# Kernel tuning notes

Measured on AMD Instinct MI355X. Metric: run time of the kernel, lower is better.

The kernel has to match this reference:

```python
import jax, jax.numpy as jnp
import numpy as np

N_NODES = 50000
N_EDGES = 1600000
NUM_REL = 4
IN_F = 256
OUT_F = 128


def setup_inputs() -> dict:
    key = jax.random.key(0)
    k1, k2, k3 = jax.random.split(key, 3)
    X = jax.random.normal(k1, (N_NODES, IN_F), dtype=jnp.float32)
    # Glorot-ish scale for the per-relation GraphConv weights
    W = jax.random.normal(k2, (NUM_REL, IN_F, OUT_F), dtype=jnp.float32) * (1.0 / np.sqrt(IN_F))
    edge_index = jax.random.randint(k3, (NUM_REL, 2, N_EDGES), 0, N_NODES, dtype=jnp.int64 if jax.config.jax_enable_x64 else jnp.int32)
    return {"X": X, "W": W, "edge_index": edge_index}


def _graph_conv(X, Wr, src, dst, n_nodes):
    """DGL GraphConv, norm='both', bias=False, allow_zero_in_degree=True."""
    ones = jnp.ones(src.shape, dtype=X.dtype)
    out_deg = jax.ops.segment_sum(ones, src, num_segments=n_nodes)
    in_deg = jax.ops.segment_sum(ones, dst, num_segments=n_nodes)
    out_norm = jnp.clip(out_deg, 1.0, None) ** -0.5  # [N]
    in_norm = jnp.clip(in_deg, 1.0, None) ** -0.5    # [N]
    # in_feats > out_feats: apply weight first (same math, cheaper messages)
    h = (X * out_norm[:, None]) @ Wr                 # [N, out]
    agg = jax.ops.segment_sum(h[src], dst, num_segments=n_nodes)  # [N, out]
    return agg * in_norm[:, None]


def reference(X, W, edge_index):
    n_nodes = X.shape[0]
    num_rel = W.shape[0]
    Z = jnp.zeros((n_nodes, W.shape[2]), dtype=X.dtype)
    for r in range(num_rel):  # small fixed loop over relations
        Z = Z + _graph_conv(X, W[r], edge_index[r, 0], edge_index[r, 1], n_nodes)
    return Z
```

## Files before the change

### kernel.cpp

```cpp
#include <hip/hip_runtime.h>

#define IN_F 256
#define OUT_F 128
#define NUM_REL 4
#define BN 64
#define PBX 64
#define PT 512

typedef unsigned int u32;
typedef unsigned short u16;
typedef unsigned char u8;

typedef __attribute__((ext_vector_type(8))) short bf16x8;
typedef __attribute__((ext_vector_type(4))) float f32x4;

static __device__ __forceinline__ u16 f32_to_bf16(float f) {
    union { float f; u32 u; } c; c.f = f;
    u32 u = c.u;
    u32 r = (u + 0x7fffu + ((u >> 16) & 1u)) >> 16;
    return (u16)r;
}
static __device__ __forceinline__ float bf16lo(u32 v) {
    union { u32 u; float f; } c; c.u = v << 16; return c.f;
}
static __device__ __forceinline__ float bf16hi(u32 v) {
    union { u32 u; float f; } c; c.u = v & 0xffff0000u; return c.f;
}

__global__ __launch_bounds__(PT) void p1_hist(const int* __restrict__ EI, u32* __restrict__ ghd,
                                              u32* __restrict__ ghs, int E, int NB, int r0) {
    int rr = blockIdx.y, x = blockIdx.x;
    int r = r0 + rr;
    const int* src = EI + (size_t)(2 * r) * E;
    const int* dst = src + E;
    extern __shared__ u32 sh[];
    u32* hd = sh; u32* hs = sh + NB;
    for (int i = threadIdx.x; i < 2 * NB; i += PT) sh[i] = 0;
    __syncthreads();
    int CH = (E + PBX - 1) / PBX;
    int lo = x * CH, hi = min(E, lo + CH);
    for (int e = lo + threadIdx.x; e < hi; e += PT) {
        atomicAdd(&hd[dst[e] >> 6], 1u);
        atomicAdd(&hs[src[e] >> 6], 1u);
    }
    __syncthreads();
    for (int b = threadIdx.x; b < NB; b += PT) {
        ghd[(size_t)(rr * NB + b) * PBX + x] = hd[b];
        ghs[(size_t)(rr * NB + b) * PBX + x] = hs[b];
    }
}

__global__ __launch_bounds__(256) void p2a_scan(u32* __restrict__ ghd, u32* __restrict__ ghs,
                                                u32* __restrict__ bintot, int BINS) {
    int wid = blockIdx.x * 4 + (threadIdx.x >> 6);
    int lane = threadIdx.x & 63;
    if (wid >= 2 * BINS) return;
    u32* g = (wid < BINS) ? ghd : ghs;
    int bin = (wid < BINS) ? wid : wid - BINS;
    u32 c = g[(size_t)bin * PBX + lane];
    u32 xv = c;
    #pragma unroll
    for (int s = 1; s < 64; s <<= 1) {
        u32 y = __shfl_up(xv, s);
        if (lane >= s) xv += y;
    }
    g[(size_t)bin * PBX + lane] = xv - c;
    if (lane == 63) bintot[wid] = xv;
}

__global__ __launch_bounds__(1024) void p2b_scan(const u32* __restrict__ bintot,
                                                 u32* __restrict__ binbase_d,
                                                 u32* __restrict__ binbase_s, int BINS) {
    __shared__ u32 s[1024];
    __shared__ u32 carry;
    int t = threadIdx.x;
    for (int seg = 0; seg < 2; seg++) {
        const u32* in = bintot + (size_t)seg * BINS;
        u32* out = seg ? binbase_s : binbase_d;
        if (t == 0) carry = 0;
        __syncthreads();
        for (int base = 0; base < BINS; base += 1024) {
            int i = base + t;
            u32 v = (i < BINS) ? in[i] : 0;
            s[t] = v;
            __syncthreads();
            for (int off = 1; off < 1024; off <<= 1) {
                u32 x = (t >= off) ? s[t - off] : 0;
                __syncthreads();
                s[t] += x;
                __syncthreads();
            }
            u32 incl = s[t]; u32 c0 = carry;
            if (i < BINS) out[i] = c0 + incl - v;
            __syncthreads();
            if (t == 1023) carry = c0 + incl;
            __syncthreads();
        }
        if (t == 0) out[BINS] = carry;
        __syncthreads();
    }
}

__global__ __launch_bounds__(PT) void p3_scatter(const int* __restrict__ EI,
                                                 const u32* __restrict__ ghd, const u32* __restrict__ ghs,
                                                 const u32* __restrict__ binbase_d, const u32* __restrict__ binbase_s,
                                                 u32* __restrict__ part_dst, u8* __restrict__ part_src,
                                                 int E, int NB, int r0) {
    int rr = blockIdx.y, x = blockIdx.x;
    int r = r0 + rr;
    const int* src = EI + (size_t)(2 * r) * E;
    const int* dst = src + E;
    extern __shared__ u32 sh[];
    u32* base_d = sh; u32* cur_d = sh + NB; u32* base_s = sh + 2 * NB; u32* cur_s = sh + 3 * NB;
    for (int b = threadIdx.x; b < NB; b += PT) {
        int bin = rr * NB + b;
        base_d[b] = binbase_d[bin] + ghd[(size_t)bin * PBX + x];
        base_s[b] = binbase_s[bin] + ghs[(size_t)bin * PBX + x];
        cur_d[b] = 0; cur_s[b] = 0;
    }
    __syncthreads();
    int CH = (E + PBX - 1) / PBX;
    int lo = x * CH, hi = min(E, lo + CH);
    for (int e = lo + threadIdx.x; e < hi; e += PT) {
        int sv = src[e], dv = dst[e];
        int db = dv >> 6, sb = sv >> 6;
        u32 rk = atomicAdd(&cur_d[db], 1u);
        part_dst[base_d[db] + rk] = ((u32)sv << 6) | (u32)(dv & 63);
        u32 rk2 = atomicAdd(&cur_s[sb], 1u);
        part_src[base_s[sb] + rk2] = (u8)(sv & 63);
    }
}

__global__ __launch_bounds__(256) void srccount_kernel(const u8* __restrict__ part_src,
                                                       const u32* __restrict__ binbase_s,
                                                       float* __restrict__ out_norm, int N, int NB) {
    int b = blockIdx.x, rr = blockIdx.y;
    int bin = rr * NB + b;
    __shared__ u32 cnt[BN];
    int t = threadIdx.x;
    if (t < BN) cnt[t] = 0;
    __syncthreads();
    u32 lo = binbase_s[bin], hi = binbase_s[bin + 1];
    for (u32 i = lo + t; i < hi; i += 256) atomicAdd(&cnt[part_src[i]], 1u);
    __syncthreads();
    if (t < BN) {
        int node = b * BN + t;
        if (node < N) out_norm[(size_t)rr * N + node] = rsqrtf((float)max(cnt[t], 1u));
    }
}

__global__ __launch_bounds__(256) void p4_sort(const u32* __restrict__ part_dst,
                                               const u32* __restrict__ binbase_d,
                                               u32* __restrict__ offs, u16* __restrict__ sorted,
                                               int N, int NB, int nrel) {
    int b = blockIdx.x, rr = blockIdx.y;
    int bin = rr * NB + b;
    __shared__ u32 cnt[BN];
    int t = threadIdx.x;
    if (t < BN) cnt[t] = 0;
    __syncthreads();
    u32 lo = binbase_d[bin], hi = binbase_d[bin + 1];
    for (u32 i = lo + t; i < hi; i += 256) atomicAdd(&cnt[part_dst[i] & 63u], 1u);
    __syncthreads();
    if (t < BN) {
        u32 c = cnt[t];
        u32 x = c;
        #pragma unroll
        for (int s = 1; s < 64; s <<= 1) {
            u32 y = __shfl_up(x, s);
            if (t >= s) x += y;
        }
        u32 excl = x - c;
        int node = b * BN + t;
        if (node < N) offs[(size_t)rr * N + node] = lo + excl;
        cnt[t] = excl;
    }
    __syncthreads();
    for (u32 i = lo + t; i < hi; i += 256) {
        u32 p = part_dst[i];
        u32 pos = atomicAdd(&cnt[p & 63u], 1u);
        sorted[lo + pos] = (u16)(p >> 6);
    }
    if (b == 0 && rr == 0 && t == 0)
        offs[(size_t)nrel * N] = binbase_d[(size_t)nrel * NB];
}

__global__ void wt_kernel(const float* __restrict__ W, u16* __restrict__ BImg, int nrel) {
    int idx = blockIdx.x * 256 + threadIdx.x;
    if (idx >= nrel * 4096) return;
    int r = idx >> 12, q = idx & 4095;
    int ng = q >> 9, kg = (q >> 4) & 31, c = q & 15;
    const float* Wr = W + (size_t)r * IN_F * OUT_F;
    u16 o[8];
    #pragma unroll
    for (int j = 0; j < 8; j++)
        o[j] = f32_to_bf16(Wr[(size_t)(8 * kg + j) * OUT_F + 16 * ng + c]);
    *(uint4*)(BImg + (size_t)idx * 8) = *(const uint4*)o;
}

__global__ void xb_kernel(const float* __restrict__ X, u16* __restrict__ Xb, int N, int nchunks) {
    int idx = blockIdx.x * 256 + threadIdx.x;
    if (idx >= nchunks) return;
    int ci = idx & 1023;
    int S = (idx >> 10) & 3;
    int R = idx >> 12;
    int mg = ci >> 7, kgl = (ci >> 4) & 7, rw = ci & 15;
    int row = R * 128 + mg * 16 + rw;
    int k0 = S * 64 + kgl * 8;
    u16 o[8] = {0, 0, 0, 0, 0, 0, 0, 0};
    if (row < N) {
        const float* xp = X + (size_t)row * IN_F + k0;
        float4 v0 = *(const float4*)xp;
        float4 v1 = *(const float4*)(xp + 4);
        o[0] = f32_to_bf16(v0.x); o[1] = f32_to_bf16(v0.y);
        o[2] = f32_to_bf16(v0.z); o[3] = f32_to_bf16(v0.w);
        o[4] = f32_to_bf16(v1.x); o[5] = f32_to_bf16(v1.y);
        o[6] = f32_to_bf16(v1.z); o[7] = f32_to_bf16(v1.w);
    }
    *(uint4*)(Xb + (size_t)idx * 8) = *(const uint4*)o;
}

__global__ __launch_bounds__(256) void gemm_kernel(const u16* __restrict__ Xb,
                                                   const u16* __restrict__ BImg,
                                                   const float* __restrict__ out_norm,
                                                   u16* __restrict__ h, int N, int r0) {
    int rr = blockIdx.y;
    int r = r0 + rr;
    int R = blockIdx.x;
    int row0 = R * 128;
    __shared__ short Alds[8192];
    __shared__ short Blds[32768];
    int t = threadIdx.x;
    int lane = t & 63, w = t >> 6;
    int wm = w >> 1, wn = w & 1;

    const uint4* bsrc = (const uint4*)(BImg + (size_t)r * 32768);
    uint4* bdst = (uint4*)Blds;
    #pragma unroll
    for (int i = 0; i < 16; i++) bdst[i * 256 + t] = bsrc[i * 256 + t];

    f32x4 acc[4][4];
    #pragma unroll
    for (int mi = 0; mi < 4; mi++)
        #pragma unroll
        for (int ni = 0; ni < 4; ni++) acc[mi][ni] = (f32x4){0.f, 0.f, 0.f, 0.f};

    const uint4* xb4 = (const uint4*)Xb + (size_t)R * 4096;
    uint4 areg[4];
    #pragma unroll
    for (int i = 0; i < 4; i++) areg[i] = xb4[i * 256 + t];

    for (int S = 0; S < 4; S++) {
        uint4* adst = (uint4*)Alds;
        #pragma unroll
        for (int i = 0; i < 4; i++) adst[i * 256 + t] = areg[i];
        __syncthreads();
        if (S < 3) {
            #pragma unroll
            for (int i = 0; i < 4; i++) areg[i] = xb4[(size_t)(S + 1) * 1024 + i * 256 + t];
        }
        #pragma unroll
        for (int kf = 0; kf < 2; kf++) {
            bf16x8 a[4], b[4];
            #pragma unroll
            for (int mi = 0; mi < 4; mi++)
                a[mi] = *(const bf16x8*)(Alds + (wm * 4 + mi) * 1024 + kf * 512 + lane * 8);
            #pragma unroll
            for (int ni = 0; ni < 4; ni++)
                b[ni] = *(const bf16x8*)(Blds + (wn * 4 + ni) * 4096 + S * 1024 + kf * 512 + lane * 8);
            #pragma unroll
            for (int mi = 0; mi < 4; mi++)
                #pragma unroll
                for (int ni = 0; ni < 4; ni++)
                    acc[mi][ni] = __builtin_amdgcn_mfma_f32_16x16x32_bf16(a[mi], b[ni], acc[mi][ni], 0, 0, 0);
        }
        __syncthreads();
    }

    const float* nrm = out_norm + (size_t)rr * N;
    u16* hr = h + (size_t)rr * N * OUT_F;
    #pragma unroll
    for (int mi = 0; mi < 4; mi++) {
        #pragma unroll
        for (int rg = 0; rg < 4; rg++) {
            int row = row0 + wm * 64 + mi * 16 + (lane >> 4) * 4 + rg;
            if (row >= N) continue;
            float nv = nrm[row];
            #pragma unroll
            for (int ni = 0; ni < 4; ni++) {
                int col = wn * 64 + ni * 16 + (lane & 15);
                hr[(size_t)row * OUT_F + col] = f32_to_bf16(acc[mi][ni][rg] * nv);
            }
        }
    }
}

__global__ __launch_bounds__(256) void aggregate_kernel(const u16* __restrict__ sorted,
                                                        const u32* __restrict__ offs,
                                                        const u16* __restrict__ h,
                                                        float* __restrict__ Z,
                                                        int N, int nrel, int accflag) {
    int wid = (blockIdx.x * 256 + threadIdx.x) >> 6;
    int lane = threadIdx.x & 63;
    int g = lane >> 4, l16 = lane & 15;
    int dst = wid * 4 + g;
    int dstc = (dst < N) ? dst : (N - 1);
    float t[8] = {0.f, 0.f, 0.f, 0.f, 0.f, 0.f, 0.f, 0.f};
    for (int rr = 0; rr < nrel; rr++) {
        u32 b = offs[(size_t)rr * N + dstc];
        u32 e = offs[(size_t)rr * N + dstc + 1];
        u32 cnt = (dst < N) ? (e - b) : 0u;
        const uint4* hr = (const uint4*)(h + (size_t)rr * N * OUT_F);
        float a[8] = {0.f, 0.f, 0.f, 0.f, 0.f, 0.f, 0.f, 0.f};
        u32 j = 0;
        for (; j + 8 <= cnt; j += 8) {
            u32 ids[8];
            #pragma unroll
            for (int q = 0; q < 8; q++) ids[q] = (u32)sorted[b + j + q];
            uint4 rv[8];
            #pragma unroll
            for (int q = 0; q < 8; q++) rv[q] = hr[(size_t)ids[q] * 16 + l16];
            #pragma unroll
            for (int q = 0; q < 8; q++) {
                a[0] += bf16lo(rv[q].x); a[1] += bf16hi(rv[q].x);
                a[2] += bf16lo(rv[q].y); a[3] += bf16hi(rv[q].y);
                a[4] += bf16lo(rv[q].z); a[5] += bf16hi(rv[q].z);
                a[6] += bf16lo(rv[q].w); a[7] += bf16hi(rv[q].w);
            }
        }
        for (; j < cnt; j++) {
            uint4 rv = hr[(size_t)sorted[b + j] * 16 + l16];
            a[0] += bf16lo(rv.x); a[1] += bf16hi(rv.x);
            a[2] += bf16lo(rv.y); a[3] += bf16hi(rv.y);
            a[4] += bf16lo(rv.z); a[5] += bf16hi(rv.z);
            a[6] += bf16lo(rv.w); a[7] += bf16hi(rv.w);
        }
        float inr = rsqrtf((float)max(cnt, 1u));
        #pragma unroll
        for (int k = 0; k < 8; k++) t[k] += inr * a[k];
    }
    if (dst < N) {
        float4* zp = (float4*)(Z + (size_t)dst * OUT_F + l16 * 8);
        if (accflag) {
            float4 z0 = zp[0], z1 = zp[1];
            z0.x += t[0]; z0.y += t[1]; z0.z += t[2]; z0.w += t[3];
            z1.x += t[4]; z1.y += t[5]; z1.z += t[6]; z1.w += t[7];
            zp[0] = z0; zp[1] = z1;
        } else {
            zp[0] = make_float4(t[0], t[1], t[2], t[3]);
            zp[1] = make_float4(t[4], t[5], t[6], t[7]);
        }
    }
}

extern "C" void kernel_launch(void* const* d_in, const int* in_sizes, int n_in,
                              void* d_out, int out_size, void* d_ws, size_t ws_size,
                              hipStream_t stream) {
    const float* X = (const float*)d_in[0];
    const float* W = (const float*)d_in[1];
    const int* EI = (const int*)d_in[2];
    float* Z = (float*)d_out;
    const int N = in_sizes[0] / IN_F;
    const int E = in_sizes[2] / (NUM_REL * 2);
    const int NB = (N + BN - 1) / BN;
    const int RBcnt = (N + 127) / 128;

    size_t sorted_o, offs_o, out_norm_o, bbd_o, bbs_o, xb_o, bimg_o, h_o,
           ghd_o, ghs_o, bintot_o, part_dst_o, part_src_o;
    auto layout = [&](int nb) -> size_t {
        size_t cur = 0;
        auto alloc = [&](size_t bytes) {
            size_t o = cur; cur = (cur + bytes + 255) & ~(size_t)255; return o;
        };
        int BINS = nb * NB;
        size_t TE = (size_t)nb * E;
        sorted_o   = alloc(TE * 2);
        offs_o     = alloc(((size_t)nb * N + 1) * 4);
        out_norm_o = alloc((size_t)nb * N * 4);
        bbd_o      = alloc((size_t)(BINS + 1) * 4);
        bbs_o      = alloc((size_t)(BINS + 1) * 4);
        xb_o       = alloc((size_t)RBcnt * 4096 * 16);
        bimg_o     = alloc((size_t)NUM_REL * 4096 * 16);
        h_o        = alloc((size_t)nb * N * OUT_F * 2);
        size_t hend = cur;
        size_t ov = h_o;
        auto oalloc = [&](size_t bytes) {
            size_t o = ov; ov = (ov + bytes + 255) & ~(size_t)255; return o;
        };
        ghd_o      = oalloc((size_t)BINS * PBX * 4);
        ghs_o      = oalloc((size_t)BINS * PBX * 4);
        bintot_o   = oalloc((size_t)2 * BINS * 4);
        part_dst_o = oalloc(TE * 4);
        part_src_o = oalloc(TE);
        return (ov > hend) ? ov : hend;
    };
    int nb = NUM_REL;
    while (nb > 1 && layout(nb) > ws_size) nb >>= 1;
    layout(nb);
    char* ws = (char*)d_ws;
    const int nbatches = (NUM_REL + nb - 1) / nb;

    u16* xb = (u16*)(ws + xb_o);
    u16* bimg = (u16*)(ws + bimg_o);

    int nchunks = RBcnt * 4096;
    xb_kernel<<<(nchunks + 255) / 256, 256, 0, stream>>>(X, xb, N, nchunks);
    wt_kernel<<<(NUM_REL * 4096 + 255) / 256, 256, 0, stream>>>(W, bimg, NUM_REL);

    if (nbatches > 1)
        hipMemsetAsync(d_out, 0, (size_t)N * OUT_F * sizeof(float), stream);

    for (int r0 = 0; r0 < NUM_REL; r0 += nb) {
        int cur = min(nb, NUM_REL - r0);
        int BINS = cur * NB;
        u16* sorted   = (u16*)(ws + sorted_o);
        u32* offs     = (u32*)(ws + offs_o);
        float* out_norm = (float*)(ws + out_norm_o);
        u32* bbd      = (u32*)(ws + bbd_o);
        u32* bbs      = (u32*)(ws + bbs_o);
        u16* h        = (u16*)(ws + h_o);
        u32* ghd      = (u32*)(ws + ghd_o);
        u32* ghs      = (u32*)(ws + ghs_o);
        u32* bintot   = (u32*)(ws + bintot_o);
        u32* part_dst = (u32*)(ws + part_dst_o);
        u8* part_src  = (u8*)(ws + part_src_o);

        p1_hist<<<dim3(PBX, cur), PT, 2 * NB * 4, stream>>>(EI, ghd, ghs, E, NB, r0);
        p2a_scan<<<(2 * BINS + 3) / 4, 256, 0, stream>>>(ghd, ghs, bintot, BINS);
        p2b_scan<<<1, 1024, 0, stream>>>(bintot, bbd, bbs, BINS);
        p3_scatter<<<dim3(PBX, cur), PT, 4 * NB * 4, stream>>>(
            EI, ghd, ghs, bbd, bbs, part_dst, part_src, E, NB, r0);
        srccount_kernel<<<dim3(NB, cur), 256, 0, stream>>>(part_src, bbs, out_norm, N, NB);
        p4_sort<<<dim3(NB, cur), 256, 0, stream>>>(part_dst, bbd, offs, sorted, N, NB, cur);
        gemm_kernel<<<dim3(RBcnt, cur), 256, 0, stream>>>(xb, bimg, out_norm, h, N, r0);
        aggregate_kernel<<<(N + 15) / 16, 256, 0, stream>>>(
            sorted, offs, h, Z, N, cur, (nbatches > 1) ? 1 : 0);
    }
}
```

Before: 461.5 us.

## Vectorize edge passes, fuse prep/srccount kernels, warp-scan, dynamic aggregate scheduling

Several independent changes land together. The histogram and scatter passes now read edges as int4, and the single-block scan switches from a shared-memory Hillis-Steele loop to wave shuffles. The source-degree count is folded into the sort kernel, and the X and W bf16 conversions are merged into one prep kernel, cutting launches. The aggregation kernel becomes persistent, pulling 4-node groups from an atomic work counter that is reset by a memset before each launch. This balances uneven degree counts but adds one atomic per group and an extra memset.

```diff
diff --git a/kernel.cpp b/kernel.cpp
--- a/kernel.cpp
+++ b/kernel.cpp
@@ -37,11 +37,22 @@
     u32* hd = sh; u32* hs = sh + NB;
     for (int i = threadIdx.x; i < 2 * NB; i += PT) sh[i] = 0;
     __syncthreads();
-    int CH = (E + PBX - 1) / PBX;
+    int CH = (((E + PBX - 1) / PBX) + 3) & ~3;
     int lo = x * CH, hi = min(E, lo + CH);
-    for (int e = lo + threadIdx.x; e < hi; e += PT) {
-        atomicAdd(&hd[dst[e] >> 6], 1u);
-        atomicAdd(&hs[src[e] >> 6], 1u);
+    if ((E & 3) == 0) {
+        for (int e = lo + (int)threadIdx.x * 4; e < hi; e += PT * 4) {
+            int4 s4 = *(const int4*)(src + e);
+            int4 d4 = *(const int4*)(dst + e);
+            atomicAdd(&hd[d4.x >> 6], 1u); atomicAdd(&hs[s4.x >> 6], 1u);
+            atomicAdd(&hd[d4.y >> 6], 1u); atomicAdd(&hs[s4.y >> 6], 1u);
+            atomicAdd(&hd[d4.z >> 6], 1u); atomicAdd(&hs[s4.z >> 6], 1u);
+            atomicAdd(&hd[d4.w >> 6], 1u); atomicAdd(&hs[s4.w >> 6], 1u);
+        }
+    } else {
+        for (int e = lo + threadIdx.x; e < hi; e += PT) {
+            atomicAdd(&hd[dst[e] >> 6], 1u);
+            atomicAdd(&hs[src[e] >> 6], 1u);
+        }
     }
     __syncthreads();
     for (int b = threadIdx.x; b < NB; b += PT) {
@@ -71,9 +82,10 @@
 __global__ __launch_bounds__(1024) void p2b_scan(const u32* __restrict__ bintot,
                                                  u32* __restrict__ binbase_d,
                                                  u32* __restrict__ binbase_s, int BINS) {
-    __shared__ u32 s[1024];
+    __shared__ u32 wsum[16];
     __shared__ u32 carry;
     int t = threadIdx.x;
+    int lane = t & 63, wv = t >> 6;
     for (int seg = 0; seg < 2; seg++) {
         const u32* in = bintot + (size_t)seg * BINS;
         u32* out = seg ? binbase_s : binbase_d;
@@ -82,15 +94,27 @@
         for (int base = 0; base < BINS; base += 1024) {
             int i = base + t;
             u32 v = (i < BINS) ? in[i] : 0;
-            s[t] = v;
+            u32 x = v;
+            #pragma unroll
+            for (int s = 1; s < 64; s <<= 1) {
+                u32 y = __shfl_up(x, s);
+                if (lane >= s) x += y;
+            }
+            if (lane == 63) wsum[wv] = x;
             __syncthreads();
-            for (int off = 1; off < 1024; off <<= 1) {
-                u32 x = (t >= off) ? s[t - off] : 0;
-                __syncthreads();
-                s[t] += x;
-                __syncthreads();
-            }
-            u32 incl = s[t]; u32 c0 = carry;
+            if (wv == 0 && lane < 16) {
+                u32 wx = wsum[lane];
+                #pragma unroll
+                for (int s = 1; s < 16; s <<= 1) {
+                    u32 wy = __shfl_up(wx, s);
+                    if (lane >= s) wx += wy;
+                }
+                wsum[lane] = wx;
+            }
+            __syncthreads();
+            u32 woff = (wv > 0) ? wsum[wv - 1] : 0;
+            u32 incl = x + woff;
+            u32 c0 = carry;
             if (i < BINS) out[i] = c0 + incl - v;
             __syncthreads();
             if (t == 1023) carry = c0 + incl;
@@ -119,39 +143,40 @@
         cur_d[b] = 0; cur_s[b] = 0;
     }
     __syncthreads();
-    int CH = (E + PBX - 1) / PBX;
+    int CH = (((E + PBX - 1) / PBX) + 3) & ~3;
     int lo = x * CH, hi = min(E, lo + CH);
-    for (int e = lo + threadIdx.x; e < hi; e += PT) {
-        int sv = src[e], dv = dst[e];
-        int db = dv >> 6, sb = sv >> 6;
-        u32 rk = atomicAdd(&cur_d[db], 1u);
-        part_dst[base_d[db] + rk] = ((u32)sv << 6) | (u32)(dv & 63);
-        u32 rk2 = atomicAdd(&cur_s[sb], 1u);
-        part_src[base_s[sb] + rk2] = (u8)(sv & 63);
-    }
-}
-
-__global__ __launch_bounds__(256) void srccount_kernel(const u8* __restrict__ part_src,
-                                                       const u32* __restrict__ binbase_s,
-                                                       float* __restrict__ out_norm, int N, int NB) {
-    int b = blockIdx.x, rr = blockIdx.y;
-    int bin = rr * NB + b;
-    __shared__ u32 cnt[BN];
-    int t = threadIdx.x;
-    if (t < BN) cnt[t] = 0;
-    __syncthreads();
-    u32 lo = binbase_s[bin], hi = binbase_s[bin + 1];
-    for (u32 i = lo + t; i < hi; i += 256) atomicAdd(&cnt[part_src[i]], 1u);
-    __syncthreads();
-    if (t < BN) {
-        int node = b * BN + t;
-        if (node < N) out_norm[(size_t)rr * N + node] = rsqrtf((float)max(cnt[t], 1u));
+    if ((E & 3) == 0) {
+        for (int e = lo + (int)threadIdx.x * 4; e < hi; e += PT * 4) {
+            int4 s4 = *(const int4*)(src + e);
+            int4 d4 = *(const int4*)(dst + e);
+            #pragma unroll
+            for (int k = 0; k < 4; k++) {
+                int sv = (&s4.x)[k], dv = (&d4.x)[k];
+                int db = dv >> 6, sb = sv >> 6;
+                u32 rk = atomicAdd(&cur_d[db], 1u);
+                part_dst[base_d[db] + rk] = ((u32)sv << 6) | (u32)(dv & 63);
+                u32 rk2 = atomicAdd(&cur_s[sb], 1u);
+                part_src[base_s[sb] + rk2] = (u8)(sv & 63);
+            }
+        }
+    } else {
+        for (int e = lo + threadIdx.x; e < hi; e += PT) {
+            int sv = src[e], dv = dst[e];
+            int db = dv >> 6, sb = sv >> 6;
+            u32 rk = atomicAdd(&cur_d[db], 1u);
+            part_dst[base_d[db] + rk] = ((u32)sv << 6) | (u32)(dv & 63);
+            u32 rk2 = atomicAdd(&cur_s[sb], 1u);
+            part_src[base_s[sb] + rk2] = (u8)(sv & 63);
+        }
     }
 }
 
 __global__ __launch_bounds__(256) void p4_sort(const u32* __restrict__ part_dst,
                                                const u32* __restrict__ binbase_d,
+                                               const u8* __restrict__ part_src,
+                                               const u32* __restrict__ binbase_s,
                                                u32* __restrict__ offs, u16* __restrict__ sorted,
+                                               float* __restrict__ out_norm,
                                                int N, int NB, int nrel) {
     int b = blockIdx.x, rr = blockIdx.y;
     int bin = rr * NB + b;
@@ -159,6 +184,17 @@
     int t = threadIdx.x;
     if (t < BN) cnt[t] = 0;
     __syncthreads();
+    {
+        u32 slo = binbase_s[bin], shi = binbase_s[bin + 1];
+        for (u32 i = slo + t; i < shi; i += 256) atomicAdd(&cnt[part_src[i]], 1u);
+    }
+    __syncthreads();
+    if (t < BN) {
+        int node = b * BN + t;
+        if (node < N) out_norm[(size_t)rr * N + node] = rsqrtf((float)max(cnt[t], 1u));
+        cnt[t] = 0;
+    }
+    __syncthreads();
     u32 lo = binbase_d[bin], hi = binbase_d[bin + 1];
     for (u32 i = lo + t; i < hi; i += 256) atomicAdd(&cnt[part_dst[i] & 63u], 1u);
     __syncthreads();
@@ -185,39 +221,39 @@
         offs[(size_t)nrel * N] = binbase_d[(size_t)nrel * NB];
 }
 
-__global__ void wt_kernel(const float* __restrict__ W, u16* __restrict__ BImg, int nrel) {
+__global__ void prep_kernel(const float* __restrict__ X, const float* __restrict__ W,
+                            u16* __restrict__ Xb, u16* __restrict__ BImg,
+                            int N, int nxb, int nwt) {
     int idx = blockIdx.x * 256 + threadIdx.x;
-    if (idx >= nrel * 4096) return;
-    int r = idx >> 12, q = idx & 4095;
-    int ng = q >> 9, kg = (q >> 4) & 31, c = q & 15;
-    const float* Wr = W + (size_t)r * IN_F * OUT_F;
-    u16 o[8];
-    #pragma unroll
-    for (int j = 0; j < 8; j++)
-        o[j] = f32_to_bf16(Wr[(size_t)(8 * kg + j) * OUT_F + 16 * ng + c]);
-    *(uint4*)(BImg + (size_t)idx * 8) = *(const uint4*)o;
-}
-
-__global__ void xb_kernel(const float* __restrict__ X, u16* __restrict__ Xb, int N, int nchunks) {
-    int idx = blockIdx.x * 256 + threadIdx.x;
-    if (idx >= nchunks) return;
-    int ci = idx & 1023;
-    int S = (idx >> 10) & 3;
-    int R = idx >> 12;
-    int mg = ci >> 7, kgl = (ci >> 4) & 7, rw = ci & 15;
-    int row = R * 128 + mg * 16 + rw;
-    int k0 = S * 64 + kgl * 8;
-    u16 o[8] = {0, 0, 0, 0, 0, 0, 0, 0};
-    if (row < N) {
-        const float* xp = X + (size_t)row * IN_F + k0;
-        float4 v0 = *(const float4*)xp;
-        float4 v1 = *(const float4*)(xp + 4);
-        o[0] = f32_to_bf16(v0.x); o[1] = f32_to_bf16(v0.y);
-        o[2] = f32_to_bf16(v0.z); o[3] = f32_to_bf16(v0.w);
-        o[4] = f32_to_bf16(v1.x); o[5] = f32_to_bf16(v1.y);
-        o[6] = f32_to_bf16(v1.z); o[7] = f32_to_bf16(v1.w);
-    }
-    *(uint4*)(Xb + (size_t)idx * 8) = *(const uint4*)o;
+    if (idx < nxb) {
+        int ci = idx & 1023;
+        int S = (idx >> 10) & 3;
+        int R = idx >> 12;
+        int mg = ci >> 7, kgl = (ci >> 4) & 7, rw = ci & 15;
+        int row = R * 128 + mg * 16 + rw;
+        int k0 = S * 64 + kgl * 8;
+        u16 o[8] = {0, 0, 0, 0, 0, 0, 0, 0};
+        if (row < N) {
+            const float* xp = X + (size_t)row * IN_F + k0;
+            float4 v0 = *(const float4*)xp;
+            float4 v1 = *(const float4*)(xp + 4);
+            o[0] = f32_to_bf16(v0.x); o[1] = f32_to_bf16(v0.y);
+            o[2] = f32_to_bf16(v0.z); o[3] = f32_to_bf16(v0.w);
+            o[4] = f32_to_bf16(v1.x); o[5] = f32_to_bf16(v1.y);
+            o[6] = f32_to_bf16(v1.z); o[7] = f32_to_bf16(v1.w);
+        }
+        *(uint4*)(Xb + (size_t)idx * 8) = *(const uint4*)o;
+    } else if (idx < nxb + nwt) {
+        int wi = idx - nxb;
+        int r = wi >> 12, q = wi & 4095;
+        int ng = q >> 9, kg = (q >> 4) & 31, c = q & 15;
+        const float* Wr = W + (size_t)r * IN_F * OUT_F;
+        u16 o[8];
+        #pragma unroll
+        for (int j = 0; j < 8; j++)
+            o[j] = f32_to_bf16(Wr[(size_t)(8 * kg + j) * OUT_F + 16 * ng + c]);
+        *(uint4*)(BImg + (size_t)wi * 8) = *(const uint4*)o;
+    }
 }
 
 __global__ __launch_bounds__(256) void gemm_kernel(const u16* __restrict__ Xb,
@@ -299,56 +335,63 @@
                                                         const u32* __restrict__ offs,
                                                         const u16* __restrict__ h,
                                                         float* __restrict__ Z,
+                                                        u32* __restrict__ qctr,
                                                         int N, int nrel, int accflag) {
-    int wid = (blockIdx.x * 256 + threadIdx.x) >> 6;
     int lane = threadIdx.x & 63;
     int g = lane >> 4, l16 = lane & 15;
-    int dst = wid * 4 + g;
-    int dstc = (dst < N) ? dst : (N - 1);
-    float t[8] = {0.f, 0.f, 0.f, 0.f, 0.f, 0.f, 0.f, 0.f};
-    for (int rr = 0; rr < nrel; rr++) {
-        u32 b = offs[(size_t)rr * N + dstc];
-        u32 e = offs[(size_t)rr * N + dstc + 1];
-        u32 cnt = (dst < N) ? (e - b) : 0u;
-        const uint4* hr = (const uint4*)(h + (size_t)rr * N * OUT_F);
-        float a[8] = {0.f, 0.f, 0.f, 0.f, 0.f, 0.f, 0.f, 0.f};
-        u32 j = 0;
-        for (; j + 8 <= cnt; j += 8) {
-            u32 ids[8];
-            #pragma unroll
-            for (int q = 0; q < 8; q++) ids[q] = (u32)sorted[b + j + q];
-            uint4 rv[8];
-            #pragma unroll
-            for (int q = 0; q < 8; q++) rv[q] = hr[(size_t)ids[q] * 16 + l16];
-            #pragma unroll
-            for (int q = 0; q < 8; q++) {
-                a[0] += bf16lo(rv[q].x); a[1] += bf16hi(rv[q].x);
-                a[2] += bf16lo(rv[q].y); a[3] += bf16hi(rv[q].y);
-                a[4] += bf16lo(rv[q].z); a[5] += bf16hi(rv[q].z);
-                a[6] += bf16lo(rv[q].w); a[7] += bf16hi(rv[q].w);
-            }
-        }
-        for (; j < cnt; j++) {
-            uint4 rv = hr[(size_t)sorted[b + j] * 16 + l16];
-            a[0] += bf16lo(rv.x); a[1] += bf16hi(rv.x);
-            a[2] += bf16lo(rv.y); a[3] += bf16hi(rv.y);
-            a[4] += bf16lo(rv.z); a[5] += bf16hi(rv.z);
-            a[6] += bf16lo(rv.w); a[7] += bf16hi(rv.w);
-        }
-        float inr = rsqrtf((float)max(cnt, 1u));
-        #pragma unroll
-        for (int k = 0; k < 8; k++) t[k] += inr * a[k];
-    }
-    if (dst < N) {
-        float4* zp = (float4*)(Z + (size_t)dst * OUT_F + l16 * 8);
-        if (accflag) {
-            float4 z0 = zp[0], z1 = zp[1];
-            z0.x += t[0]; z0.y += t[1]; z0.z += t[2]; z0.w += t[3];
-            z1.x += t[4]; z1.y += t[5]; z1.z += t[6]; z1.w += t[7];
-            zp[0] = z0; zp[1] = z1;
-        } else {
-            zp[0] = make_float4(t[0], t[1], t[2], t[3]);
-            zp[1] = make_float4(t[4], t[5], t[6], t[7]);
+    int ngroups = (N + 3) >> 2;
+    for (;;) {
+        u32 gidx = 0;
+        if (lane == 0) gidx = atomicAdd(qctr, 1u);
+        gidx = (u32)__shfl((int)gidx, 0);
+        if (gidx >= (u32)ngroups) break;
+        int dst = (int)gidx * 4 + g;
+        int dstc = (dst < N) ? dst : (N - 1);
+        float t[8] = {0.f, 0.f, 0.f, 0.f, 0.f, 0.f, 0.f, 0.f};
+        for (int rr = 0; rr < nrel; rr++) {
+            u32 b = offs[(size_t)rr * N + dstc];
+            u32 e = offs[(size_t)rr * N + dstc + 1];
+            u32 cnt = (dst < N) ? (e - b) : 0u;
+            const uint4* hr = (const uint4*)(h + (size_t)rr * N * OUT_F);
+            float a[8] = {0.f, 0.f, 0.f, 0.f, 0.f, 0.f, 0.f, 0.f};
+            u32 j = 0;
+            for (; j + 8 <= cnt; j += 8) {
+                u32 ids[8];
+                #pragma unroll
+                for (int q = 0; q < 8; q++) ids[q] = (u32)sorted[b + j + q];
+                uint4 rv[8];
+                #pragma unroll
+                for (int q = 0; q < 8; q++) rv[q] = hr[(size_t)ids[q] * 16 + l16];
+                #pragma unroll
+                for (int q = 0; q < 8; q++) {
+                    a[0] += bf16lo(rv[q].x); a[1] += bf16hi(rv[q].x);
+                    a[2] += bf16lo(rv[q].y); a[3] += bf16hi(rv[q].y);
+                    a[4] += bf16lo(rv[q].z); a[5] += bf16hi(rv[q].z);
+                    a[6] += bf16lo(rv[q].w); a[7] += bf16hi(rv[q].w);
+                }
+            }
+            for (; j < cnt; j++) {
+                uint4 rv = hr[(size_t)sorted[b + j] * 16 + l16];
+                a[0] += bf16lo(rv.x); a[1] += bf16hi(rv.x);
+                a[2] += bf16lo(rv.y); a[3] += bf16hi(rv.y);
+                a[4] += bf16lo(rv.z); a[5] += bf16hi(rv.z);
+                a[6] += bf16lo(rv.w); a[7] += bf16hi(rv.w);
+            }
+            float inr = rsqrtf((float)max(cnt, 1u));
+            #pragma unroll
+            for (int k = 0; k < 8; k++) t[k] += inr * a[k];
+        }
+        if (dst < N) {
+            float4* zp = (float4*)(Z + (size_t)dst * OUT_F + l16 * 8);
+            if (accflag) {
+                float4 z0 = zp[0], z1 = zp[1];
+                z0.x += t[0]; z0.y += t[1]; z0.z += t[2]; z0.w += t[3];
+                z1.x += t[4]; z1.y += t[5]; z1.z += t[6]; z1.w += t[7];
+                zp[0] = z0; zp[1] = z1;
+            } else {
+                zp[0] = make_float4(t[0], t[1], t[2], t[3]);
+                zp[1] = make_float4(t[4], t[5], t[6], t[7]);
+            }
         }
     }
 }
@@ -365,7 +408,7 @@
     const int NB = (N + BN - 1) / BN;
     const int RBcnt = (N + 127) / 128;
 
-    size_t sorted_o, offs_o, out_norm_o, bbd_o, bbs_o, xb_o, bimg_o, h_o,
+    size_t sorted_o, offs_o, out_norm_o, bbd_o, bbs_o, qctr_o, xb_o, bimg_o, h_o,
            ghd_o, ghs_o, bintot_o, part_dst_o, part_src_o;
     auto layout = [&](int nb) -> size_t {
         size_t cur = 0;
@@ -379,6 +422,7 @@
         out_norm_o = alloc((size_t)nb * N * 4);
         bbd_o      = alloc((size_t)(BINS + 1) * 4);
         bbs_o      = alloc((size_t)(BINS + 1) * 4);
+        qctr_o     = alloc(256);
         xb_o       = alloc((size_t)RBcnt * 4096 * 16);
         bimg_o     = alloc((size_t)NUM_REL * 4096 * 16);
         h_o        = alloc((size_t)nb * N * OUT_F * 2);
@@ -402,10 +446,11 @@
 
     u16* xb = (u16*)(ws + xb_o);
     u16* bimg = (u16*)(ws + bimg_o);
-
-    int nchunks = RBcnt * 4096;
-    xb_kernel<<<(nchunks + 255) / 256, 256, 0, stream>>>(X, xb, N, nchunks);
-    wt_kernel<<<(NUM_REL * 4096 + 255) / 256, 256, 0, stream>>>(W, bimg, NUM_REL);
+    u32* qctr = (u32*)(ws + qctr_o);
+
+    int nxb = RBcnt * 4096;
+    int nwt = NUM_REL * 4096;
+    prep_kernel<<<(nxb + nwt + 255) / 256, 256, 0, stream>>>(X, W, xb, bimg, N, nxb, nwt);
 
     if (nbatches > 1)
         hipMemsetAsync(d_out, 0, (size_t)N * OUT_F * sizeof(float), stream);
@@ -430,10 +475,13 @@
         p2b_scan<<<1, 1024, 0, stream>>>(bintot, bbd, bbs, BINS);
         p3_scatter<<<dim3(PBX, cur), PT, 4 * NB * 4, stream>>>(
             EI, ghd, ghs, bbd, bbs, part_dst, part_src, E, NB, r0);
-        srccount_kernel<<<dim3(NB, cur), 256, 0, stream>>>(part_src, bbs, out_norm, N, NB);
-        p4_sort<<<dim3(NB, cur), 256, 0, stream>>>(part_dst, bbd, offs, sorted, N, NB, cur);
+        p4_sort<<<dim3(NB, cur), 256, 0, stream>>>(
+            part_dst, bbd, part_src, bbs, offs, sorted, out_norm, N, NB, cur);
         gemm_kernel<<<dim3(RBcnt, cur), 256, 0, stream>>>(xb, bimg, out_norm, h, N, r0);
-        aggregate_kernel<<<(N + 15) / 16, 256, 0, stream>>>(
-            sorted, offs, h, Z, N, cur, (nbatches > 1) ? 1 : 0);
-    }
-}
+        hipMemsetAsync(qctr, 0, 4, stream);
+        int ngroups = (N + 3) >> 2;
+        int ablocks = min(2048, max(1, ngroups));
+        aggregate_kernel<<<ablocks, 256, 0, stream>>>(
+            sorted, offs, h, Z, qctr, N, cur, (nbatches > 1) ? 1 : 0);
+    }
+}
```

New measurement: 602.2 us. +30.5%, slower.
